# Performance work log

Hardware: AMD Instinct MI355X
Metric: run time of the kernel (lower is better)

The kernel has to match this reference:

```python
import jax, jax.numpy as jnp
import numpy as np

SIGMA = 5.0  # matches init_kwargs sigma


def so3_exp_map(w):
    """Rodrigues formula. w: [..., 3] axis-angle -> [..., 3, 3] rotation."""
    theta = jnp.sqrt(jnp.sum(w * w, axis=-1) + 1e-12)            # [...]
    wx, wy, wz = w[..., 0], w[..., 1], w[..., 2]
    z = jnp.zeros_like(wx)
    # normalized skew matrix K = hat(w) / theta
    K = jnp.stack([z, -wz, wy,
                   wz, z, -wx,
                   -wy, wx, z], axis=-1).reshape(w.shape[:-1] + (3, 3))
    K = K / theta[..., None, None]
    s = jnp.sin(theta)[..., None, None]
    c = (1.0 - jnp.cos(theta))[..., None, None]
    I = jnp.eye(3, dtype=w.dtype)
    return I + s * K + c * (K @ K)


def setup_inputs() -> dict:
    key = jax.random.key(0)
    k1, k2, k3, k4, k5 = jax.random.split(key, 5)
    P, N, E = 65536, 512, 4096
    # spread points/control points over a volume where sigma=5 is a meaningful scale
    points = jax.random.normal(k1, (P, 3), dtype=jnp.float32) * 10.0
    control_points = jax.random.normal(k2, (N, 3), dtype=jnp.float32) * 10.0
    rot_vec = jax.random.normal(k3, (N, 3), dtype=jnp.float32) * 0.1
    t = jax.random.normal(k4, (N, 3), dtype=jnp.float32) * 0.1
    edges = jax.random.randint(k5, (E, 2), 0, N, dtype=jnp.int64)
    return {"points": points, "control_points": control_points,
            "rot_vec": rot_vec, "t": t, "edges": edges}


def reference(points, control_points, rot_vec, t, edges):
    # ---- warp_points ----
    # local: [P, N, 3]
    local = points[:, None, :] - control_points[None, :, :]
    skin = jnp.exp(-jnp.sum(local * local, axis=-1) / (2.0 * SIGMA * SIGMA))  # [P, N]
    skin = skin / (jnp.sum(skin, axis=-1, keepdims=True) + 1e-5)
    R = so3_exp_map(rot_vec)                                    # [N, 3, 3]
    warped = (jnp.einsum('nij,pnj->pni', R, local)
              + t[None, :, :] + control_points[None, :, :])     # [P, N, 3]
    warped = jnp.sum(warped * skin[..., None], axis=1)          # [P, 3]
    # ---- reg_term ----
    i, j = edges[:, 0], edges[:, 1]
    ci, cj = control_points[i], control_points[j]               # [E, 3]
    ti, tj = t[i], t[j]
    Ri = R[i]                                                   # [E, 3, 3]
    resid = jnp.einsum('mij,mj->mi', Ri, cj - ci) + ci + ti - (cj + tj)
    reg = jnp.sum(resid * resid)
    return warped, reg
```

## Files before the change

kernel.cpp:

```cpp
#include <hip/hip_runtime.h>
#include <math.h>


constexpr int NP = 65536;
constexpr int NN = 512;
constexpr int NE = 4096;
constexpr int PPT = 4;
constexpr int CH = 16;
constexpr int TPC = 64;
constexpr int PPB = TPC * PPT;
constexpr int NPC = NN / CH;
constexpr float KEXP = -0.02f * 1.44269504088896340736f;
constexpr float M2K = -2.0f * KEXP;

#if defined(__has_builtin)
#if __has_builtin(__builtin_amdgcn_exp2f)
#define FAST_EXP2(x) __builtin_amdgcn_exp2f(x)
#endif
#endif
#ifndef FAST_EXP2
#define FAST_EXP2(x) exp2f(x)
#endif

__device__ __forceinline__ void rodrigues(float wx, float wy, float wz, float* R) {
    float t2 = wx * wx + wy * wy + wz * wz + 1e-12f;
    float th = sqrtf(t2);
    float inv = 1.0f / th;
    float kx = wx * inv, ky = wy * inv, kz = wz * inv;
    float s = sinf(th);
    float c = 1.0f - cosf(th);
    float kxky = kx * ky, kxkz = kx * kz, kykz = ky * kz;
    R[0] = 1.0f - c * (ky * ky + kz * kz);
    R[1] = -s * kz + c * kxky;
    R[2] =  s * ky + c * kxkz;
    R[3] =  s * kz + c * kxky;
    R[4] = 1.0f - c * (kx * kx + kz * kz);
    R[5] = -s * kx + c * kykz;
    R[6] = -s * ky + c * kxkz;
    R[7] =  s * kx + c * kykz;
    R[8] = 1.0f - c * (kx * kx + ky * ky);
}

__global__ __launch_bounds__(1024) void deform_kernel(
    const float* __restrict__ points,
    const float* __restrict__ cps,
    const float* __restrict__ rot,
    const float* __restrict__ tr,
    const int* __restrict__ edges,
    float* __restrict__ out)
{
    __shared__ float nd[NN * 16];
    __shared__ float4 red[CH / 2][PPB];
    __shared__ float red2[16];

    const int bid = blockIdx.x;
    const int tid = threadIdx.x;

    if (bid < NP / PPB) {
        if (tid < NN) {
            int n = tid;
            float R[9];
            rodrigues(rot[3 * n + 0], rot[3 * n + 1], rot[3 * n + 2], R);
            float cx = cps[3 * n + 0], cy = cps[3 * n + 1], cz = cps[3 * n + 2];
            float tx = tr[3 * n + 0], ty = tr[3 * n + 1], tz = tr[3 * n + 2];
            float bx = tx + cx - (R[0] * cx + R[1] * cy + R[2] * cz);
            float by = ty + cy - (R[3] * cx + R[4] * cy + R[5] * cz);
            float bz = tz + cz - (R[6] * cx + R[7] * cy + R[8] * cz);
            float kc2 = KEXP * (cx * cx + cy * cy + cz * cz);
            float* r = &nd[n * 16];
            r[0] = R[0]; r[1] = R[1]; r[2] = R[2]; r[3] = R[3];
            r[4] = R[4]; r[5] = R[5]; r[6] = R[6]; r[7] = R[7];
            r[8] = R[8]; r[9] = bx;  r[10] = by;  r[11] = bz;
            r[12] = cx;  r[13] = cy; r[14] = cz;  r[15] = kc2;
        }
        __syncthreads();

        const int chunk = tid >> 6;
        const int tslot = tid & 63;
        const int p0 = bid * PPB + tslot * PPT;

        const float4* pv = (const float4*)(points + 3 * p0);
        float4 va = pv[0], vb = pv[1], vc = pv[2];
        float px[PPT] = {va.x, va.w, vb.z, vc.y};
        float py[PPT] = {va.y, vb.x, vb.w, vc.z};
        float pz[PPT] = {va.z, vb.y, vc.x, vc.w};
        float kp2[PPT];
        #pragma unroll
        for (int k = 0; k < PPT; ++k)
            kp2[k] = KEXP * (px[k] * px[k] + py[k] * py[k] + pz[k] * pz[k]);

        float ax[PPT] = {0,0,0,0}, ay[PPT] = {0,0,0,0}, az[PPT] = {0,0,0,0}, ws[PPT] = {0,0,0,0};
        const float* base = &nd[chunk * NPC * 16];

        #pragma unroll 2
        for (int n = 0; n < NPC; ++n) {
            const float4* q = (const float4*)(base + n * 16);
            float4 q0 = q[0];
            float4 q1 = q[1];
            float4 q2 = q[2];
            float4 q3 = q[3];
            #pragma unroll
            for (int k = 0; k < PPT; ++k) {
                float dot = fmaf(q3.x, px[k], fmaf(q3.y, py[k], q3.z * pz[k]));
                float w = FAST_EXP2(fmaf(M2K, dot, kp2[k] + q3.w));
                float yx = fmaf(q0.x, px[k], fmaf(q0.y, py[k], fmaf(q0.z, pz[k], q2.y)));
                float yy = fmaf(q0.w, px[k], fmaf(q1.x, py[k], fmaf(q1.y, pz[k], q2.z)));
                float yz = fmaf(q1.z, px[k], fmaf(q1.w, py[k], fmaf(q2.x, pz[k], q2.w)));
                ws[k] += w;
                ax[k] = fmaf(w, yx, ax[k]);
                ay[k] = fmaf(w, yy, ay[k]);
                az[k] = fmaf(w, yz, az[k]);
            }
        }

        #pragma unroll
        for (int s = CH / 2; s >= 1; s >>= 1) {
            if (chunk >= s && chunk < 2 * s) {
                #pragma unroll
                for (int k = 0; k < PPT; ++k)
                    red[chunk - s][tslot * PPT + k] = make_float4(ax[k], ay[k], az[k], ws[k]);
            }
            __syncthreads();
            if (chunk < s) {
                #pragma unroll
                for (int k = 0; k < PPT; ++k) {
                    float4 v = red[chunk][tslot * PPT + k];
                    ax[k] += v.x; ay[k] += v.y; az[k] += v.z; ws[k] += v.w;
                }
            }
            __syncthreads();
        }

        if (chunk == 0) {
            float o[12];
            #pragma unroll
            for (int k = 0; k < PPT; ++k) {
                float invw = 1.0f / (ws[k] + 1e-5f);
                o[3 * k + 0] = ax[k] * invw;
                o[3 * k + 1] = ay[k] * invw;
                o[3 * k + 2] = az[k] * invw;
            }
            float4* ov = (float4*)(out + 3 * p0);
            ov[0] = make_float4(o[0], o[1], o[2], o[3]);
            ov[1] = make_float4(o[4], o[5], o[6], o[7]);
            ov[2] = make_float4(o[8], o[9], o[10], o[11]);
        }
    } else {
        float acc = 0.0f;
        for (int e = tid; e < NE; e += 1024) {
            int i = edges[2 * e + 0];
            int j = edges[2 * e + 1];
            float R[9];
            rodrigues(rot[3 * i + 0], rot[3 * i + 1], rot[3 * i + 2], R);
            float cix = cps[3 * i + 0], ciy = cps[3 * i + 1], ciz = cps[3 * i + 2];
            float cjx = cps[3 * j + 0], cjy = cps[3 * j + 1], cjz = cps[3 * j + 2];
            float dx = cjx - cix, dy = cjy - ciy, dz = cjz - ciz;
            float rx = fmaf(R[0], dx, fmaf(R[1], dy, R[2] * dz)) + cix + tr[3 * i + 0] - cjx - tr[3 * j + 0];
            float ry = fmaf(R[3], dx, fmaf(R[4], dy, R[5] * dz)) + ciy + tr[3 * i + 1] - cjy - tr[3 * j + 1];
            float rz = fmaf(R[6], dx, fmaf(R[7], dy, R[8] * dz)) + ciz + tr[3 * i + 2] - cjz - tr[3 * j + 2];
            acc += rx * rx + ry * ry + rz * rz;
        }
        #pragma unroll
        for (int off = 32; off > 0; off >>= 1)
            acc += __shfl_down(acc, off, 64);
        int wid = tid >> 6;
        if ((tid & 63) == 0) red2[wid] = acc;
        __syncthreads();
        if (tid == 0) {
            float s = 0.0f;
            #pragma unroll
            for (int i = 0; i < 16; ++i) s += red2[i];
            out[3 * NP] = s;
        }
    }
}

extern "C" void kernel_launch(void* const* d_in, const int* in_sizes, int n_in,
                              void* d_out, int out_size, void* d_ws, size_t ws_size,
                              hipStream_t stream) {
    const float* points = (const float*)d_in[0];
    const float* cps    = (const float*)d_in[1];
    const float* rot    = (const float*)d_in[2];
    const float* tr     = (const float*)d_in[3];
    const int*   edges  = (const int*)d_in[4];
    float* out = (float*)d_out;
    deform_kernel<<<NP / PPB + 1, 1024, 0, stream>>>(points, cps, rot, tr, edges, out);
}
```

Before: 85.94 us.

## Flatten chunk reduction, fold scale into control points, distribute reg term across blocks

Replaces the log-step shared-memory tree reduction, which used several barriers, with a single write-then-sum pass by chunk 0. It folds the M2K scale into the stored control-point coordinates to remove one multiply per inner iteration, and raises the inner unroll from 2 to 4. It drops the extra serial block for the regularization term. Instead each block computes 16 edges from the shared per-node table and adds its partial with atomicAdd. That atomic assumes the output scalar starts at zero, which nothing in the kernel guarantees.

```diff
diff --git a/kernel.cpp b/kernel.cpp
--- a/kernel.cpp
+++ b/kernel.cpp
@@ -4,11 +4,9 @@
 
 constexpr int NP = 65536;
 constexpr int NN = 512;
-constexpr int NE = 4096;
+constexpr int PPB = 256;
 constexpr int PPT = 4;
 constexpr int CH = 16;
-constexpr int TPC = 64;
-constexpr int PPB = TPC * PPT;
 constexpr int NPC = NN / CH;
 constexpr float KEXP = -0.02f * 1.44269504088896340736f;
 constexpr float M2K = -2.0f * KEXP;
@@ -50,128 +48,113 @@
     float* __restrict__ out)
 {
     __shared__ float nd[NN * 16];
-    __shared__ float4 red[CH / 2][PPB];
-    __shared__ float red2[16];
+    __shared__ float4 red[CH - 1][PPT][64];
 
     const int bid = blockIdx.x;
     const int tid = threadIdx.x;
 
-    if (bid < NP / PPB) {
-        if (tid < NN) {
-            int n = tid;
-            float R[9];
-            rodrigues(rot[3 * n + 0], rot[3 * n + 1], rot[3 * n + 2], R);
-            float cx = cps[3 * n + 0], cy = cps[3 * n + 1], cz = cps[3 * n + 2];
-            float tx = tr[3 * n + 0], ty = tr[3 * n + 1], tz = tr[3 * n + 2];
-            float bx = tx + cx - (R[0] * cx + R[1] * cy + R[2] * cz);
-            float by = ty + cy - (R[3] * cx + R[4] * cy + R[5] * cz);
-            float bz = tz + cz - (R[6] * cx + R[7] * cy + R[8] * cz);
-            float kc2 = KEXP * (cx * cx + cy * cy + cz * cz);
-            float* r = &nd[n * 16];
-            r[0] = R[0]; r[1] = R[1]; r[2] = R[2]; r[3] = R[3];
-            r[4] = R[4]; r[5] = R[5]; r[6] = R[6]; r[7] = R[7];
-            r[8] = R[8]; r[9] = bx;  r[10] = by;  r[11] = bz;
-            r[12] = cx;  r[13] = cy; r[14] = cz;  r[15] = kc2;
+    if (tid < NN) {
+        const int n = tid;
+        float R[9];
+        rodrigues(rot[3 * n + 0], rot[3 * n + 1], rot[3 * n + 2], R);
+        float cx = cps[3 * n + 0], cy = cps[3 * n + 1], cz = cps[3 * n + 2];
+        float tx = tr[3 * n + 0], ty = tr[3 * n + 1], tz = tr[3 * n + 2];
+        float bx = tx + cx - (R[0] * cx + R[1] * cy + R[2] * cz);
+        float by = ty + cy - (R[3] * cx + R[4] * cy + R[5] * cz);
+        float bz = tz + cz - (R[6] * cx + R[7] * cy + R[8] * cz);
+        float kc2 = KEXP * (cx * cx + cy * cy + cz * cz);
+        float4* r = (float4*)(&nd[n * 16]);
+        r[0] = make_float4(R[0], R[1], R[2], R[3]);
+        r[1] = make_float4(R[4], R[5], R[6], R[7]);
+        r[2] = make_float4(R[8], bx, by, bz);
+        r[3] = make_float4(M2K * cx, M2K * cy, M2K * cz, kc2);
+    }
+    __syncthreads();
+
+    const int tslot = tid & 63;
+    const int chunk = tid >> 6;
+    const int p0 = bid * PPB + tslot * PPT;
+
+    const float4* pv = (const float4*)(points + 3 * p0);
+    float4 va = pv[0], vb = pv[1], vc = pv[2];
+    float px[PPT] = {va.x, va.w, vb.z, vc.y};
+    float py[PPT] = {va.y, vb.x, vb.w, vc.z};
+    float pz[PPT] = {va.z, vb.y, vc.x, vc.w};
+    float kp2[PPT];
+    #pragma unroll
+    for (int k = 0; k < PPT; ++k)
+        kp2[k] = KEXP * (px[k] * px[k] + py[k] * py[k] + pz[k] * pz[k]);
+
+    float ax[PPT] = {0, 0, 0, 0}, ay[PPT] = {0, 0, 0, 0};
+    float az[PPT] = {0, 0, 0, 0}, ws[PPT] = {0, 0, 0, 0};
+    const float* base = &nd[chunk * NPC * 16];
+
+    #pragma unroll 4
+    for (int n = 0; n < NPC; ++n) {
+        const float4* q = (const float4*)(base + n * 16);
+        float4 q0 = q[0];
+        float4 q1 = q[1];
+        float4 q2 = q[2];
+        float4 q3 = q[3];
+        #pragma unroll
+        for (int k = 0; k < PPT; ++k) {
+            float tk = kp2[k] + q3.w;
+            float arg = fmaf(q3.x, px[k], fmaf(q3.y, py[k], fmaf(q3.z, pz[k], tk)));
+            float w = FAST_EXP2(arg);
+            float yx = fmaf(q0.x, px[k], fmaf(q0.y, py[k], fmaf(q0.z, pz[k], q2.y)));
+            float yy = fmaf(q0.w, px[k], fmaf(q1.x, py[k], fmaf(q1.y, pz[k], q2.z)));
+            float yz = fmaf(q1.z, px[k], fmaf(q1.w, py[k], fmaf(q2.x, pz[k], q2.w)));
+            ws[k] += w;
+            ax[k] = fmaf(w, yx, ax[k]);
+            ay[k] = fmaf(w, yy, ay[k]);
+            az[k] = fmaf(w, yz, az[k]);
         }
-        __syncthreads();
+    }
 
-        const int chunk = tid >> 6;
-        const int tslot = tid & 63;
-        const int p0 = bid * PPB + tslot * PPT;
-
-        const float4* pv = (const float4*)(points + 3 * p0);
-        float4 va = pv[0], vb = pv[1], vc = pv[2];
-        float px[PPT] = {va.x, va.w, vb.z, vc.y};
-        float py[PPT] = {va.y, vb.x, vb.w, vc.z};
-        float pz[PPT] = {va.z, vb.y, vc.x, vc.w};
-        float kp2[PPT];
+    if (chunk != 0) {
         #pragma unroll
         for (int k = 0; k < PPT; ++k)
-            kp2[k] = KEXP * (px[k] * px[k] + py[k] * py[k] + pz[k] * pz[k]);
+            red[chunk - 1][k][tslot] = make_float4(ax[k], ay[k], az[k], ws[k]);
+    }
+    __syncthreads();
 
-        float ax[PPT] = {0,0,0,0}, ay[PPT] = {0,0,0,0}, az[PPT] = {0,0,0,0}, ws[PPT] = {0,0,0,0};
-        const float* base = &nd[chunk * NPC * 16];
-
-        #pragma unroll 2
-        for (int n = 0; n < NPC; ++n) {
-            const float4* q = (const float4*)(base + n * 16);
-            float4 q0 = q[0];
-            float4 q1 = q[1];
-            float4 q2 = q[2];
-            float4 q3 = q[3];
+    if (chunk == 0) {
+        #pragma unroll 4
+        for (int r = 0; r < CH - 1; ++r) {
             #pragma unroll
             for (int k = 0; k < PPT; ++k) {
-                float dot = fmaf(q3.x, px[k], fmaf(q3.y, py[k], q3.z * pz[k]));
-                float w = FAST_EXP2(fmaf(M2K, dot, kp2[k] + q3.w));
-                float yx = fmaf(q0.x, px[k], fmaf(q0.y, py[k], fmaf(q0.z, pz[k], q2.y)));
-                float yy = fmaf(q0.w, px[k], fmaf(q1.x, py[k], fmaf(q1.y, pz[k], q2.z)));
-                float yz = fmaf(q1.z, px[k], fmaf(q1.w, py[k], fmaf(q2.x, pz[k], q2.w)));
-                ws[k] += w;
-                ax[k] = fmaf(w, yx, ax[k]);
-                ay[k] = fmaf(w, yy, ay[k]);
-                az[k] = fmaf(w, yz, az[k]);
+                float4 v = red[r][k][tslot];
+                ax[k] += v.x; ay[k] += v.y; az[k] += v.z; ws[k] += v.w;
             }
         }
-
+        float o[12];
         #pragma unroll
-        for (int s = CH / 2; s >= 1; s >>= 1) {
-            if (chunk >= s && chunk < 2 * s) {
-                #pragma unroll
-                for (int k = 0; k < PPT; ++k)
-                    red[chunk - s][tslot * PPT + k] = make_float4(ax[k], ay[k], az[k], ws[k]);
-            }
-            __syncthreads();
-            if (chunk < s) {
-                #pragma unroll
-                for (int k = 0; k < PPT; ++k) {
-                    float4 v = red[chunk][tslot * PPT + k];
-                    ax[k] += v.x; ay[k] += v.y; az[k] += v.z; ws[k] += v.w;
-                }
-            }
-            __syncthreads();
+        for (int k = 0; k < PPT; ++k) {
+            float invw = 1.0f / (ws[k] + 1e-5f);
+            o[3 * k + 0] = ax[k] * invw;
+            o[3 * k + 1] = ay[k] * invw;
+            o[3 * k + 2] = az[k] * invw;
         }
-
-        if (chunk == 0) {
-            float o[12];
-            #pragma unroll
-            for (int k = 0; k < PPT; ++k) {
-                float invw = 1.0f / (ws[k] + 1e-5f);
-                o[3 * k + 0] = ax[k] * invw;
-                o[3 * k + 1] = ay[k] * invw;
-                o[3 * k + 2] = az[k] * invw;
-            }
-            float4* ov = (float4*)(out + 3 * p0);
-            ov[0] = make_float4(o[0], o[1], o[2], o[3]);
-            ov[1] = make_float4(o[4], o[5], o[6], o[7]);
-            ov[2] = make_float4(o[8], o[9], o[10], o[11]);
-        }
-    } else {
-        float acc = 0.0f;
-        for (int e = tid; e < NE; e += 1024) {
-            int i = edges[2 * e + 0];
-            int j = edges[2 * e + 1];
-            float R[9];
-            rodrigues(rot[3 * i + 0], rot[3 * i + 1], rot[3 * i + 2], R);
-            float cix = cps[3 * i + 0], ciy = cps[3 * i + 1], ciz = cps[3 * i + 2];
-            float cjx = cps[3 * j + 0], cjy = cps[3 * j + 1], cjz = cps[3 * j + 2];
-            float dx = cjx - cix, dy = cjy - ciy, dz = cjz - ciz;
-            float rx = fmaf(R[0], dx, fmaf(R[1], dy, R[2] * dz)) + cix + tr[3 * i + 0] - cjx - tr[3 * j + 0];
-            float ry = fmaf(R[3], dx, fmaf(R[4], dy, R[5] * dz)) + ciy + tr[3 * i + 1] - cjy - tr[3 * j + 1];
-            float rz = fmaf(R[6], dx, fmaf(R[7], dy, R[8] * dz)) + ciz + tr[3 * i + 2] - cjz - tr[3 * j + 2];
-            acc += rx * rx + ry * ry + rz * rz;
-        }
+        float4* ov = (float4*)(out + 3 * p0);
+        ov[0] = make_float4(o[0], o[1], o[2], o[3]);
+        ov[1] = make_float4(o[4], o[5], o[6], o[7]);
+        ov[2] = make_float4(o[8], o[9], o[10], o[11]);
+    } else if (tid >= 1024 - 16) {
+        const int e = bid * 16 + (tid & 15);
+        const int i = edges[2 * e + 0];
+        const int j = edges[2 * e + 1];
+        const float4* ri = (const float4*)(&nd[i * 16]);
+        float4 q0 = ri[0], q1 = ri[1], q2 = ri[2];
+        float cjx = cps[3 * j + 0], cjy = cps[3 * j + 1], cjz = cps[3 * j + 2];
+        float tjx = tr[3 * j + 0],  tjy = tr[3 * j + 1],  tjz = tr[3 * j + 2];
+        float rx = fmaf(q0.x, cjx, fmaf(q0.y, cjy, fmaf(q0.z, cjz, q2.y))) - cjx - tjx;
+        float ry = fmaf(q0.w, cjx, fmaf(q1.x, cjy, fmaf(q1.y, cjz, q2.z))) - cjy - tjy;
+        float rz = fmaf(q1.z, cjx, fmaf(q1.w, cjy, fmaf(q2.x, cjz, q2.w))) - cjz - tjz;
+        float acc = rx * rx + ry * ry + rz * rz;
         #pragma unroll
-        for (int off = 32; off > 0; off >>= 1)
-            acc += __shfl_down(acc, off, 64);
-        int wid = tid >> 6;
-        if ((tid & 63) == 0) red2[wid] = acc;
-        __syncthreads();
-        if (tid == 0) {
-            float s = 0.0f;
-            #pragma unroll
-            for (int i = 0; i < 16; ++i) s += red2[i];
-            out[3 * NP] = s;
-        }
+        for (int off = 8; off > 0; off >>= 1)
+            acc += __shfl_down(acc, off, 16);
+        if ((tid & 15) == 0) atomicAdd(out + 3 * NP, acc);
     }
 }
 
@@ -184,5 +167,5 @@
     const float* tr     = (const float*)d_in[3];
     const int*   edges  = (const int*)d_in[4];
     float* out = (float*)d_out;
-    deform_kernel<<<NP / PPB + 1, 1024, 0, stream>>>(points, cps, rot, tr, edges, out);
+    deform_kernel<<<NP / PPB, 1024, 0, stream>>>(points, cps, rot, tr, edges, out);
 }
```

Result: faster. 81.79 us (-4.8%).
